# Optimization experiments

Hardware: AMD Instinct MI355X
Metric: run time of the kernel (lower is better)

The kernel has to match this reference:

```python
import jax, jax.numpy as jnp
import numpy as np

B, L, D, N = 2, 2048, 1024, 16
DT_MIN, DT_MAX = 1e-3, 1e-1


def setup_inputs() -> dict:
    key = jax.random.key(0)
    ks = jax.random.split(key, 8)
    u = jax.random.normal(ks[0], (B, L, D), dtype=jnp.float32)
    # torch.nn.Linear weights are (out_features, in_features)
    W_dt = jax.random.normal(ks[1], (D, D), dtype=jnp.float32) * 0.02
    b_dt = jnp.zeros((D,), dtype=jnp.float32)
    W_B = jax.random.normal(ks[2], (D * N, D), dtype=jnp.float32) * 0.02
    b_B = jnp.zeros((D * N,), dtype=jnp.float32)
    W_C = jax.random.normal(ks[3], (D * N, D), dtype=jnp.float32) * 0.02
    b_C = jnp.zeros((D * N,), dtype=jnp.float32)
    # log_A init: log(1..N) broadcast over channels (HiPPO-ish diagonal)
    log_A = jnp.broadcast_to(jnp.log(jnp.arange(1, N + 1, dtype=jnp.float32)), (D, N))
    D_skip = jnp.ones((D,), dtype=jnp.float32)
    lo, hi = float(np.log(DT_MIN)), float(np.log(DT_MAX))
    dt_bias = jax.random.uniform(ks[4], (D,), dtype=jnp.float32) * (hi - lo) + lo
    return {"u": u, "log_A": log_A, "D_skip": D_skip, "dt_bias": dt_bias,
            "W_dt": W_dt, "b_dt": b_dt, "W_B": W_B, "b_B": b_B,
            "W_C": W_C, "b_C": b_C}


def reference(u, log_A, D_skip, dt_bias, W_dt, b_dt, W_B, b_B, W_C, b_C):
    b, l, d = u.shape
    n = log_A.shape[1]
    A = -jnp.exp(log_A)                                   # (d, n), A < 0
    # token-dependent parameters, computed for all timesteps at once
    dt = jax.nn.softplus(u @ W_dt.T + b_dt + dt_bias)     # (b, l, d)
    Bt = (u @ W_B.T + b_B).reshape(b, l, d, n)            # (b, l, d, n)
    Ct = (u @ W_C.T + b_C).reshape(b, l, d, n)            # (b, l, d, n)
    # exact ZOH discretisation
    A_bar = jnp.exp(dt[..., None] * A)                    # (b, l, d, n)
    B_bar = (A_bar - 1.0) / A * Bt                        # (b, l, d, n)
    x_in = B_bar * u[..., None]                           # (b, l, d, n)
    # recurrent scan over time
    def step(h, inp):
        a_t, x_t, c_t = inp                               # each (b, d, n)
        h = a_t * h + x_t
        y_t = jnp.sum(c_t * h, axis=-1)                   # (b, d)
        return h, y_t
    h0 = jnp.zeros((b, d, n), dtype=u.dtype)
    xs = (jnp.moveaxis(A_bar, 1, 0), jnp.moveaxis(x_in, 1, 0), jnp.moveaxis(Ct, 1, 0))
    _, ys = jax.lax.scan(step, h0, xs)                    # ys: (l, b, d)
    y = jnp.moveaxis(ys, 0, 1) + D_skip * u               # (b, l, d)
    return y
```

## Files before the change

kernel.cpp:

```cpp
#include <hip/hip_runtime.h>
#include <hip/hip_bf16.h>
#include <stdint.h>

constexpr int Bb = 2;
constexpr int Ll = 2048;
constexpr int Dd = 1024;
constexpr int Nn = 16;
constexpr int NB = Dd * Nn;
constexpr int SL = 64;
constexpr int NCH = Bb * Dd;
constexpr int KCAT = 3 * Dd;

typedef __bf16 bf16_t;
typedef __bf16 bf16x8 __attribute__((ext_vector_type(8)));
typedef __bf16 bf16x4 __attribute__((ext_vector_type(4)));
typedef float f32x4 __attribute__((ext_vector_type(4)));

__device__ inline void gld_lds16(const void* g, void* l) {
    __builtin_amdgcn_global_load_lds(
        (const __attribute__((address_space(1))) unsigned int*)g,
        (__attribute__((address_space(3))) unsigned int*)l, 16, 0, 0);
}

__global__ __launch_bounds__(256) void cvt_bf16(const float* __restrict__ s,
                                                bf16_t* __restrict__ d, int n4) {
    int i = blockIdx.x * 256 + threadIdx.x;
    const int stride = gridDim.x * 256;
    const float4* s4 = (const float4*)s;
    bf16x4* d4 = (bf16x4*)d;
    for (; i < n4; i += stride) {
        float4 v = s4[i];
        bf16x4 o = {(bf16_t)v.x, (bf16_t)v.y, (bf16_t)v.z, (bf16_t)v.w};
        d4[i] = o;
    }
}

__global__ __launch_bounds__(256) void build_ucat(const float* __restrict__ u,
                                                  bf16_t* __restrict__ ucat) {
    const int i = blockIdx.x * 256 + threadIdx.x;
    const int row = i >> 8;
    const int c = (i & 255) << 2;
    float4 v = ((const float4*)u)[i];
    bf16x4 hi = {(bf16_t)v.x, (bf16_t)v.y, (bf16_t)v.z, (bf16_t)v.w};
    bf16x4 lo = {(bf16_t)(v.x - (float)hi.x), (bf16_t)(v.y - (float)hi.y),
                 (bf16_t)(v.z - (float)hi.z), (bf16_t)(v.w - (float)hi.w)};
    bf16_t* r = ucat + (size_t)row * KCAT;
    *(bf16x4*)(r + c) = hi;
    *(bf16x4*)(r + Dd + c) = lo;
    *(bf16x4*)(r + 2 * Dd + c) = hi;
}

__global__ __launch_bounds__(256) void build_wcat(const float* __restrict__ w,
                                                  bf16_t* __restrict__ wcat) {
    const int i = blockIdx.x * 256 + threadIdx.x;
    const int row = i >> 8;
    const int c = (i & 255) << 2;
    float4 v = ((const float4*)w)[i];
    bf16x4 hi = {(bf16_t)v.x, (bf16_t)v.y, (bf16_t)v.z, (bf16_t)v.w};
    bf16x4 lo = {(bf16_t)(v.x - (float)hi.x), (bf16_t)(v.y - (float)hi.y),
                 (bf16_t)(v.z - (float)hi.z), (bf16_t)(v.w - (float)hi.w)};
    bf16_t* r = wcat + (size_t)row * KCAT;
    *(bf16x4*)(r + c) = hi;
    *(bf16x4*)(r + Dd + c) = hi;
    *(bf16x4*)(r + 2 * Dd + c) = lo;
}

template <int EP, typename OutT>
__global__ __launch_bounds__(256) void gemm_mfma(
    const bf16_t* __restrict__ Abase, int CL, int l0, int K,
    const bf16_t* __restrict__ W, const float* __restrict__ b1,
    const float* __restrict__ b2, OutT* __restrict__ C, int N)
{
    __shared__ bf16_t As[128 * 32];
    __shared__ bf16_t Bs[128 * 32];

    const int tid = threadIdx.x;
    const int bn = blockIdx.x * 128;
    const int rglob = blockIdx.y * 128;
    const int batch = rglob / CL;
    const int rin = rglob % CL;
    const bf16_t* Ap = Abase + ((size_t)batch * Ll + l0 + rin) * K;
    const bf16_t* Wp = W + (size_t)bn * K;
    OutT* Cp = C + (size_t)rglob * N;

    const int sr = tid >> 2;
    const int sc = (tid & 3) << 3;
    char* ldsA = (char*)As + tid * 16;
    char* ldsB = (char*)Bs + tid * 16;

    const int lane = tid & 63;
    const int wid = tid >> 6;
    const int wm = (wid & 1) << 6;
    const int wn = (wid >> 1) << 6;
    const int lr = lane & 15;
    const int lq = lane >> 4;

    f32x4 acc[4][4] = {};

    for (int k0 = 0; k0 < K; k0 += 32) {
        __syncthreads();
        gld_lds16(Ap + (size_t)sr * K + k0 + sc, ldsA);
        gld_lds16(Ap + (size_t)(sr + 64) * K + k0 + sc, ldsA + 4096);
        gld_lds16(Wp + (size_t)sr * K + k0 + sc, ldsB);
        gld_lds16(Wp + (size_t)(sr + 64) * K + k0 + sc, ldsB + 4096);
        __syncthreads();

        bf16x8 af[4], bfr[4];
#pragma unroll
        for (int mi = 0; mi < 4; ++mi)
            af[mi] = *(const bf16x8*)&As[(wm + mi * 16 + lr) * 32 + lq * 8];
#pragma unroll
        for (int ni = 0; ni < 4; ++ni)
            bfr[ni] = *(const bf16x8*)&Bs[(wn + ni * 16 + lr) * 32 + lq * 8];
#pragma unroll
        for (int mi = 0; mi < 4; ++mi)
#pragma unroll
            for (int ni = 0; ni < 4; ++ni)
                acc[mi][ni] = __builtin_amdgcn_mfma_f32_16x16x32_bf16(
                    af[mi], bfr[ni], acc[mi][ni], 0, 0, 0);
    }

#pragma unroll
    for (int ni = 0; ni < 4; ++ni) {
        const int col = bn + wn + ni * 16 + lr;
        const float bc = b1[col] + (EP == 1 ? b2[col] : 0.f);
#pragma unroll
        for (int mi = 0; mi < 4; ++mi)
#pragma unroll
            for (int i = 0; i < 4; ++i) {
                float v = acc[mi][ni][i] + bc;
                if (EP == 1) v = (v > 20.f) ? v : log1pf(__expf(v));
                Cp[(size_t)(wm + mi * 16 + lq * 4 + i) * N + col] = (OutT)v;
            }
    }
}

__global__ __launch_bounds__(256) void scan_seg_local(
    const float* __restrict__ u, const float* __restrict__ dt,
    const bf16_t* __restrict__ Bt_c, const float* __restrict__ log_A,
    float* __restrict__ pseg, float* __restrict__ hseg, int CL, int l0)
{
    const int tid = threadIdx.x;
    const int g = tid >> 4, n = tid & 15;
    const int gid = blockIdx.x * 16 + g;
    const int ch = gid & (NCH - 1);
    const int s = gid >> 11;
    const int b = ch >> 10, d = ch & (Dd - 1);

    const float A = -__expf(log_A[d * Nn + n]);
    const float rA = 1.f / A;

    size_t idx_bn = (size_t)(b * CL + s * SL) * NB + d * Nn + n;
    size_t idx_u = ((size_t)b * Ll + l0 + s * SL) * Dd + d;

    float p = 1.f, h = 0.f;
    for (int l = 0; l < SL; ++l) {
        const float dtv = dt[idx_u];
        const float uv = u[idx_u];
        const float bv = (float)Bt_c[idx_bn];
        const float a = __expf(dtv * A);
        p *= a;
        h = a * h + (a - 1.f) * rA * bv * uv;
        idx_bn += NB; idx_u += Dd;
    }
    const size_t o = ((size_t)s * NCH + ch) * Nn + n;
    pseg[o] = p;
    hseg[o] = h;
}

__global__ __launch_bounds__(256) void scan_combine(
    const float* __restrict__ pseg, const float* __restrict__ hseg,
    float* __restrict__ hin_arr, float* __restrict__ h_state,
    int NSEG, int l0)
{
    const int t = blockIdx.x * 256 + threadIdx.x;
    float hin = (l0 == 0) ? 0.f : h_state[t];
    for (int s = 0; s < NSEG; ++s) {
        const size_t o = (size_t)s * (NCH * Nn) + t;
        hin_arr[o] = hin;
        hin = pseg[o] * hin + hseg[o];
    }
    h_state[t] = hin;
}

__global__ __launch_bounds__(256) void scan_seg_final(
    const float* __restrict__ u, const float* __restrict__ dt,
    const bf16_t* __restrict__ Bt_c, const bf16_t* __restrict__ Ct_c,
    const float* __restrict__ log_A, const float* __restrict__ D_skip,
    const float* __restrict__ hin_arr, float* __restrict__ y, int CL, int l0)
{
    const int tid = threadIdx.x;
    const int g = tid >> 4, n = tid & 15;
    const int gid = blockIdx.x * 16 + g;
    const int ch = gid & (NCH - 1);
    const int s = gid >> 11;
    const int b = ch >> 10, d = ch & (Dd - 1);

    const float A = -__expf(log_A[d * Nn + n]);
    const float rA = 1.f / A;
    const float Dsk = D_skip[d];

    size_t idx_bn = (size_t)(b * CL + s * SL) * NB + d * Nn + n;
    size_t idx_u = ((size_t)b * Ll + l0 + s * SL) * Dd + d;

    float h = hin_arr[((size_t)s * NCH + ch) * Nn + n];
    for (int l = 0; l < SL; ++l) {
        const float dtv = dt[idx_u];
        const float uv = u[idx_u];
        const float bv = (float)Bt_c[idx_bn];
        const float cv = (float)Ct_c[idx_bn];
        const float a = __expf(dtv * A);
        h = a * h + (a - 1.f) * rA * bv * uv;
        float p = cv * h;
        p += __shfl_xor(p, 1);
        p += __shfl_xor(p, 2);
        p += __shfl_xor(p, 4);
        p += __shfl_xor(p, 8);
        if (n == 0) y[idx_u] = p + Dsk * uv;
        idx_bn += NB; idx_u += Dd;
    }
}

static inline size_t al256(size_t x) { return (x + 255) & ~(size_t)255; }

extern "C" void kernel_launch(void* const* d_in, const int* in_sizes, int n_in,
                              void* d_out, int out_size, void* d_ws, size_t ws_size,
                              hipStream_t stream) {
    const float* u       = (const float*)d_in[0];
    const float* log_A   = (const float*)d_in[1];
    const float* D_skip  = (const float*)d_in[2];
    const float* dt_bias = (const float*)d_in[3];
    const float* W_dt    = (const float*)d_in[4];
    const float* b_dt    = (const float*)d_in[5];
    const float* W_B     = (const float*)d_in[6];
    const float* b_B     = (const float*)d_in[7];
    const float* W_C     = (const float*)d_in[8];
    const float* b_C     = (const float*)d_in[9];
    float* y = (float*)d_out;

    const size_t sz_ubf  = al256((size_t)Bb * Ll * Dd * 2);
    const size_t sz_w    = al256((size_t)NB * Dd * 2);
    const size_t sz_h    = al256((size_t)NCH * Nn * 4);
    const size_t sz_dtf  = al256((size_t)Bb * Ll * Dd * 4);
    const size_t sz_ucat = al256((size_t)Bb * Ll * KCAT * 2);
    const size_t sz_wcat = al256((size_t)Dd * KCAT * 2);

    int CL = 128;
    const int cands[5] = {2048, 1024, 512, 256, 128};
    for (int i = 0; i < 5; ++i) {
        const int c = cands[i];
        const int nseg = c / SL;
        const size_t seg = 3 * al256((size_t)nseg * NCH * Nn * 4);
        const size_t chunk = 2 * al256((size_t)2 * c * NB * 2);
        const size_t ovl = sz_ucat + sz_wcat;
        const size_t need = sz_ubf + 2 * sz_w + sz_h + sz_dtf + seg +
                            (chunk > ovl ? chunk : ovl);
        if (need <= ws_size) { CL = c; break; }
    }
    const int NSEG = CL / SL;

    char* p = (char*)d_ws;
    bf16_t* u_bf   = (bf16_t*)p; p += sz_ubf;
    bf16_t* wB_bf  = (bf16_t*)p; p += sz_w;
    bf16_t* wC_bf  = (bf16_t*)p; p += sz_w;
    float* h_state = (float*)p; p += sz_h;
    float* dt_full = (float*)p; p += sz_dtf;
    const size_t sz_seg1 = al256((size_t)NSEG * NCH * Nn * 4);
    float* pseg    = (float*)p; p += sz_seg1;
    float* hseg    = (float*)p; p += sz_seg1;
    float* hin_arr = (float*)p; p += sz_seg1;
    char* chunk0 = p;
    bf16_t* Bt_c = (bf16_t*)chunk0;
    bf16_t* Ct_c = (bf16_t*)(chunk0 + al256((size_t)2 * CL * NB * 2));
    bf16_t* u_cat = (bf16_t*)chunk0;
    bf16_t* w_cat = (bf16_t*)(chunk0 + sz_ucat);

    cvt_bf16<<<2048, 256, 0, stream>>>(u, u_bf, Bb * Ll * Dd / 4);
    cvt_bf16<<<2048, 256, 0, stream>>>(W_B, wB_bf, NB * Dd / 4);
    cvt_bf16<<<2048, 256, 0, stream>>>(W_C, wC_bf, NB * Dd / 4);
    build_ucat<<<Bb * Ll * Dd / 4 / 256, 256, 0, stream>>>(u, u_cat);
    build_wcat<<<Dd * Dd / 4 / 256, 256, 0, stream>>>(W_dt, w_cat);

    gemm_mfma<1, float><<<dim3(Dd / 128, Bb * Ll / 128), 256, 0, stream>>>(
        u_cat, Ll, 0, KCAT, w_cat, b_dt, dt_bias, dt_full, Dd);

    for (int l0 = 0; l0 < Ll; l0 += CL) {
        gemm_mfma<0, bf16_t><<<dim3(NB / 128, 2 * CL / 128), 256, 0, stream>>>(
            u_bf, CL, l0, Dd, wB_bf, b_B, nullptr, Bt_c, NB);
        gemm_mfma<0, bf16_t><<<dim3(NB / 128, 2 * CL / 128), 256, 0, stream>>>(
            u_bf, CL, l0, Dd, wC_bf, b_C, nullptr, Ct_c, NB);
        scan_seg_local<<<dim3(128 * NSEG), 256, 0, stream>>>(
            u, dt_full, Bt_c, log_A, pseg, hseg, CL, l0);
        scan_combine<<<dim3(128), 256, 0, stream>>>(
            pseg, hseg, hin_arr, h_state, NSEG, l0);
        scan_seg_final<<<dim3(128 * NSEG), 256, 0, stream>>>(
            u, dt_full, Bt_c, Ct_c, log_A, D_skip, hin_arr, y, CL, l0);
    }
}
```

Before: 799.2 us.

## Add 256x256-tile pipelined MFMA GEMM for the B and C projections

Adds a new 512-thread GEMM kernel with 256x256 output tiles, 128KB of dynamic LDS, XOR-swizzled LDS staging through direct global-to-LDS loads, and double-buffered prefetch that issues the A tile one step ahead and the W tile two steps ahead. MFMA issue is interleaved with staged loads and raised in priority via setprio. The B and C projections, which dominate the FLOPs, use it whenever the chunk length is a multiple of 256. The goal is higher arithmetic intensity and better overlap of memory and compute, at the cost of heavy register and LDS pressure and more complex synchronisation.

```diff
diff --git a/kernel.cpp b/kernel.cpp
--- a/kernel.cpp
+++ b/kernel.cpp
@@ -132,6 +132,126 @@
                 if (EP == 1) v = (v > 20.f) ? v : log1pf(__expf(v));
                 Cp[(size_t)(wm + mi * 16 + lq * 4 + i) * N + col] = (OutT)v;
             }
+    }
+}
+
+__global__ __launch_bounds__(512, 2) void gemm256(
+    const bf16_t* __restrict__ Abase, int CL, int l0, int K,
+    const bf16_t* __restrict__ W, const float* __restrict__ b1,
+    bf16_t* __restrict__ C, int N)
+{
+    extern __shared__ char smem[];
+    const int tid = threadIdx.x;
+    const int bn = blockIdx.x * 256;
+    const int rglob = blockIdx.y * 256;
+    const int batch = rglob / CL;
+    const int rin = rglob % CL;
+    const bf16_t* Ap = Abase + ((size_t)batch * Ll + l0 + rin) * K;
+    const bf16_t* Wp = W + (size_t)bn * K;
+    bf16_t* Cp = C + (size_t)rglob * N;
+
+    const int lane = tid & 63;
+    const int wid = tid >> 6;
+    const int wr = wid >> 2;
+    const int wc = wid & 3;
+    const int lr = lane & 15;
+    const int lq = lane >> 4;
+    const int NT = K >> 6;
+
+    const int c0 = tid, c1 = tid + 512;
+    const int r0 = c0 >> 3, r1 = c1 >> 3;
+    const int kb0 = ((c0 & 7) << 3) ^ ((r0 & 7) << 3);
+    const int kb1 = ((c1 & 7) << 3) ^ ((r1 & 7) << 3);
+
+    auto stage = [&](const bf16_t* src, char* dst, int tt, int h) {
+        gld_lds16(src + (size_t)(h * 128 + r0) * K + tt * 64 + kb0,
+                  dst + h * 16384 + c0 * 16);
+        gld_lds16(src + (size_t)(h * 128 + r1) * K + tt * 64 + kb1,
+                  dst + h * 16384 + c1 * 16);
+    };
+
+    stage(Ap, smem, 0, 0);
+    stage(Ap, smem, 0, 1);
+    stage(Wp, smem + 32768, 0, 0);
+    stage(Wp, smem + 32768, 0, 1);
+    if (NT > 1) {
+        stage(Wp, smem + 65536 + 32768, 1, 0);
+        stage(Wp, smem + 65536 + 32768, 1, 1);
+        asm volatile("s_waitcnt vmcnt(4)" ::: "memory");
+    } else {
+        asm volatile("s_waitcnt vmcnt(0)" ::: "memory");
+    }
+    __builtin_amdgcn_s_barrier();
+
+    f32x4 acc[8][4] = {};
+    const int xsw = (lr & 7) << 4;
+
+    for (int t = 0; t < NT; ++t) {
+        char* Ard = smem + ((t & 1) ? 65536 : 0);
+        char* Brd = Ard + 32768;
+        char* Awr = smem + ((t & 1) ? 0 : 65536);
+        char* Bwr = Brd;
+
+        bf16x8 bfr[2][4];
+#pragma unroll
+        for (int p = 0; p < 4; ++p) {
+            if (p == 0) { if (t + 1 < NT) stage(Ap, Awr, t + 1, 0); }
+            if (p == 1) { if (t + 1 < NT) stage(Ap, Awr, t + 1, 1); }
+            if (p == 2) { if (t + 2 < NT) stage(Wp, Bwr, t + 2, 0); }
+            if (p == 3) { if (t + 2 < NT) stage(Wp, Bwr, t + 2, 1); }
+
+            if (p == 0) {
+#pragma unroll
+                for (int ks = 0; ks < 2; ++ks)
+#pragma unroll
+                    for (int ni = 0; ni < 4; ++ni)
+                        bfr[ks][ni] = *(const bf16x8*)(Brd +
+                            (wc * 64 + ni * 16 + lr) * 128 +
+                            ((ks * 64 + lq * 16) ^ xsw));
+            }
+            bf16x8 a0k0 = *(const bf16x8*)(Ard +
+                (wr * 128 + (2 * p) * 16 + lr) * 128 + ((lq * 16) ^ xsw));
+            bf16x8 a0k1 = *(const bf16x8*)(Ard +
+                (wr * 128 + (2 * p) * 16 + lr) * 128 + ((64 + lq * 16) ^ xsw));
+            bf16x8 a1k0 = *(const bf16x8*)(Ard +
+                (wr * 128 + (2 * p + 1) * 16 + lr) * 128 + ((lq * 16) ^ xsw));
+            bf16x8 a1k1 = *(const bf16x8*)(Ard +
+                (wr * 128 + (2 * p + 1) * 16 + lr) * 128 + ((64 + lq * 16) ^ xsw));
+
+            __builtin_amdgcn_s_barrier();
+            __builtin_amdgcn_s_setprio(1);
+#pragma unroll
+            for (int ni = 0; ni < 4; ++ni) {
+                acc[2 * p][ni] = __builtin_amdgcn_mfma_f32_16x16x32_bf16(
+                    a0k0, bfr[0][ni], acc[2 * p][ni], 0, 0, 0);
+                acc[2 * p][ni] = __builtin_amdgcn_mfma_f32_16x16x32_bf16(
+                    a0k1, bfr[1][ni], acc[2 * p][ni], 0, 0, 0);
+                acc[2 * p + 1][ni] = __builtin_amdgcn_mfma_f32_16x16x32_bf16(
+                    a1k0, bfr[0][ni], acc[2 * p + 1][ni], 0, 0, 0);
+                acc[2 * p + 1][ni] = __builtin_amdgcn_mfma_f32_16x16x32_bf16(
+                    a1k1, bfr[1][ni], acc[2 * p + 1][ni], 0, 0, 0);
+            }
+            __builtin_amdgcn_s_setprio(0);
+            if (p == 3) {
+                if (t + 2 < NT)
+                    asm volatile("s_waitcnt vmcnt(4)" ::: "memory");
+                else if (t + 1 < NT)
+                    asm volatile("s_waitcnt vmcnt(0)" ::: "memory");
+            }
+            __builtin_amdgcn_s_barrier();
+        }
+    }
+
+#pragma unroll
+    for (int ni = 0; ni < 4; ++ni) {
+        const int col = bn + wc * 64 + ni * 16 + lr;
+        const float bc = b1[col];
+#pragma unroll
+        for (int mi = 0; mi < 8; ++mi)
+#pragma unroll
+            for (int i = 0; i < 4; ++i)
+                Cp[(size_t)(wr * 128 + mi * 16 + lq * 4 + i) * N + col] =
+                    (bf16_t)(acc[mi][ni][i] + bc);
     }
 }
 
@@ -238,6 +358,9 @@
     const float* b_C     = (const float*)d_in[9];
     float* y = (float*)d_out;
 
+    hipFuncSetAttribute(reinterpret_cast<const void*>(gemm256),
+                        hipFuncAttributeMaxDynamicSharedMemorySize, 131072);
+
     const size_t sz_ubf  = al256((size_t)Bb * Ll * Dd * 2);
     const size_t sz_w    = al256((size_t)NB * Dd * 2);
     const size_t sz_h    = al256((size_t)NCH * Nn * 4);
@@ -284,11 +407,19 @@
     gemm_mfma<1, float><<<dim3(Dd / 128, Bb * Ll / 128), 256, 0, stream>>>(
         u_cat, Ll, 0, KCAT, w_cat, b_dt, dt_bias, dt_full, Dd);
 
+    const bool use256 = (CL % 256 == 0);
     for (int l0 = 0; l0 < Ll; l0 += CL) {
-        gemm_mfma<0, bf16_t><<<dim3(NB / 128, 2 * CL / 128), 256, 0, stream>>>(
-            u_bf, CL, l0, Dd, wB_bf, b_B, nullptr, Bt_c, NB);
-        gemm_mfma<0, bf16_t><<<dim3(NB / 128, 2 * CL / 128), 256, 0, stream>>>(
-            u_bf, CL, l0, Dd, wC_bf, b_C, nullptr, Ct_c, NB);
+        if (use256) {
+            gemm256<<<dim3(NB / 256, 2 * CL / 256), 512, 131072, stream>>>(
+                u_bf, CL, l0, Dd, wB_bf, b_B, Bt_c, NB);
+            gemm256<<<dim3(NB / 256, 2 * CL / 256), 512, 131072, stream>>>(
+                u_bf, CL, l0, Dd, wC_bf, b_C, Ct_c, NB);
+        } else {
+            gemm_mfma<0, bf16_t><<<dim3(NB / 128, 2 * CL / 128), 256, 0, stream>>>(
+                u_bf, CL, l0, Dd, wB_bf, b_B, nullptr, Bt_c, NB);
+            gemm_mfma<0, bf16_t><<<dim3(NB / 128, 2 * CL / 128), 256, 0, stream>>>(
+                u_bf, CL, l0, Dd, wC_bf, b_C, nullptr, Ct_c, NB);
+        }
         scan_seg_local<<<dim3(128 * NSEG), 256, 0, stream>>>(
             u, dt_full, Bt_c, log_A, pseg, hseg, CL, l0);
         scan_combine<<<dim3(128), 256, 0, stream>>>(
```

After: 730.5 us. 1.09x faster.
